# Optimization experiments

Measured on AMD Instinct MI355X. Metric: run time of the kernel, lower is better.

## Reference

```python
import jax, jax.numpy as jnp
import numpy as np

N_NODES = 100000
SAMPLES = 16


def setup_inputs() -> dict:
    key = jax.random.key(0)
    ks = jax.random.split(key, 9)
    x = jax.random.normal(ks[0], (N_NODES, 128), dtype=jnp.float32)
    neigh_idx = jax.random.randint(ks[1], (N_NODES, SAMPLES), 0, N_NODES)
    batch = jax.random.randint(ks[2], (8192,), 0, N_NODES)
    W1 = jax.random.normal(ks[3], (256, 128), dtype=jnp.float32) * 0.05
    b1 = jax.random.normal(ks[4], (128,), dtype=jnp.float32) * 0.05
    W2 = jax.random.normal(ks[5], (256, 128), dtype=jnp.float32) * 0.05
    b2 = jax.random.normal(ks[6], (128,), dtype=jnp.float32) * 0.05
    Wout = jax.random.normal(ks[7], (128, 64), dtype=jnp.float32) * 0.05
    bout = jax.random.normal(ks[8], (64,), dtype=jnp.float32) * 0.05
    return {"x": x, "neigh_idx": neigh_idx, "batch": batch,
            "W1": W1, "b1": b1, "W2": W2, "b2": b2,
            "Wout": Wout, "bout": bout}


def _sage_layer(h, neigh_idx, W, b):
    # h: [N, d]; gather sampled neighbors -> [N, S, d]; max-aggregate; concat-linear
    neigh = h[neigh_idx]                     # irregular gather, memory-bound core
    agg = jnp.max(neigh, axis=1)             # MaxAggregation over samples
    feats = jnp.concatenate([h, agg], axis=-1)  # [N, 2d]
    return feats @ W + b


def reference(x, neigh_idx, batch, W1, b1, W2, b2, Wout, bout):
    # layer 1: relu(Linear(concat(x, max_neigh(x))))
    h1 = jax.nn.relu(_sage_layer(x, neigh_idx, W1, b1))
    # layer 2 (== n_layers): Linear output (no relu) fed straight into proj_out
    h2 = _sage_layer(h1, neigh_idx, W2, b2)
    out = h2 @ Wout + bout                   # proj_out (Dropout is eval identity)
    return out[batch]
```

## Files before the change

kernel.cpp:

```cpp
#include <hip/hip_runtime.h>
#include <cmath>
#include <cstdint>

#define N_NODES 100000
#define SAMPLES 16
#define DIM 128
#define NBATCH 8192

#define FSTR 264
#define H2STR 132

typedef _Float16 half8 __attribute__((ext_vector_type(8)));
typedef float floatx4 __attribute__((ext_vector_type(4)));

__device__ __forceinline__ half8 h8max(half8 a, half8 b) {
    half8 r;
#pragma unroll
    for (int i = 0; i < 8; ++i) r[i] = (a[i] > b[i]) ? a[i] : b[i];
    return r;
}

__global__ __launch_bounds__(256) void setup_kernel(
    const float* __restrict__ x,
    const float* __restrict__ W1,
    const float* __restrict__ W2,
    const int* __restrict__ batch,
    const int* __restrict__ nidx,
    int* __restrict__ flags,
    _Float16* __restrict__ xh,
    _Float16* __restrict__ W1sw,
    _Float16* __restrict__ W2sw) {
    const int bid = blockIdx.x;
    if (bid < 6250) {
        const size_t base = ((size_t)bid * 256 + threadIdx.x) * 8;
        const float4* xp = (const float4*)(x + base);
        const float4 a = xp[0], b = xp[1];
        half8 v;
        v[0] = (_Float16)a.x; v[1] = (_Float16)a.y;
        v[2] = (_Float16)a.z; v[3] = (_Float16)a.w;
        v[4] = (_Float16)b.x; v[5] = (_Float16)b.y;
        v[6] = (_Float16)b.z; v[7] = (_Float16)b.w;
        *(half8*)(xh + base) = v;
    } else if (bid < 6282) {
        const int tid = (bid - 6250) * 256 + threadIdx.x;
        const int which = tid >> 12;
        const int r = tid & 4095;
        const int kb = r >> 9, nb = (r >> 6) & 7, lane = r & 63;
        const int q = lane >> 4, c = lane & 15;
        const float* W = which ? W2 : W1;
        _Float16* O = which ? W2sw : W1sw;
        const int k0 = kb * 32 + q * 8;
        const int n = nb * 16 + c;
        half8 v;
#pragma unroll
        for (int j = 0; j < 8; ++j) v[j] = (_Float16)W[(size_t)(k0 + j) * DIM + n];
        *(half8*)(O + (size_t)r * 8) = v;
    } else {
        const int j = (bid - 6282) * 256 + threadIdx.x;
        if (j < NBATCH) {
            const int b = batch[j];
            flags[b] = 1;
            const int* row = nidx + (size_t)b * SAMPLES;
#pragma unroll
            for (int s = 0; s < SAMPLES; ++s) flags[row[s]] = 1;
        }
    }
}

__global__ __launch_bounds__(256) void layer1_kernel(
    const _Float16* __restrict__ xh,
    const int* __restrict__ nidx,
    const _Float16* __restrict__ W1sw,
    const float* __restrict__ b1,
    const int* __restrict__ flags,
    _Float16* __restrict__ h1h) {
    const int t = threadIdx.x;
    const int g = t >> 4;
    const int cl = t & 15;
    const int i0 = blockIdx.x * 16;
    const int i = i0 + g;

    __shared__ __align__(16) _Float16 feats[16 * FSTR];

    const bool fi = (flags[i] == 1);
    if (fi) {
        const char* xb = (const char*)xh;
        const int cb = cl * 16;
        const half8 self = *(const half8*)(xb + (size_t)i * 256 + cb);
        const int4* ip = (const int4*)(nidx + (size_t)i * SAMPLES);
        const int4 a0 = ip[0], a1 = ip[1], a2 = ip[2], a3 = ip[3];
        int off[16];
        off[0]  = a0.x * 256 + cb; off[1]  = a0.y * 256 + cb;
        off[2]  = a0.z * 256 + cb; off[3]  = a0.w * 256 + cb;
        off[4]  = a1.x * 256 + cb; off[5]  = a1.y * 256 + cb;
        off[6]  = a1.z * 256 + cb; off[7]  = a1.w * 256 + cb;
        off[8]  = a2.x * 256 + cb; off[9]  = a2.y * 256 + cb;
        off[10] = a2.z * 256 + cb; off[11] = a2.w * 256 + cb;
        off[12] = a3.x * 256 + cb; off[13] = a3.y * 256 + cb;
        off[14] = a3.z * 256 + cb; off[15] = a3.w * 256 + cb;
        half8 v[16];
#pragma unroll
        for (int s = 0; s < 16; ++s) v[s] = *(const half8*)(xb + off[s]);
#pragma unroll
        for (int s = 0; s < 8; ++s) v[s] = h8max(v[s], v[s + 8]);
#pragma unroll
        for (int s = 0; s < 4; ++s) v[s] = h8max(v[s], v[s + 4]);
        const half8 mx = h8max(h8max(v[0], v[1]), h8max(v[2], v[3]));
        *(half8*)(feats + g * FSTR + cl * 8) = self;
        *(half8*)(feats + g * FSTR + DIM + cl * 8) = mx;
    } else {
        half8 z;
#pragma unroll
        for (int e = 0; e < 8; ++e) z[e] = (_Float16)0.f;
        *(half8*)(feats + g * FSTR + cl * 8) = z;
        *(half8*)(feats + g * FSTR + DIM + cl * 8) = z;
    }
    __syncthreads();

    const int wave = t >> 6;
    const int lane = t & 63;
    const int q = lane >> 4, c = lane & 15;
    const int nb0 = wave * 2;
    floatx4 acc[2];
    acc[0] = (floatx4){0.f, 0.f, 0.f, 0.f};
    acc[1] = (floatx4){0.f, 0.f, 0.f, 0.f};
#pragma unroll
    for (int kb = 0; kb < 8; ++kb) {
        const half8 a = *(const half8*)(feats + c * FSTR + kb * 32 + q * 8);
#pragma unroll
        for (int j = 0; j < 2; ++j) {
            const half8 b = *(const half8*)(W1sw + (size_t)((kb * 8 + nb0 + j) * 64 + lane) * 8);
            acc[j] = __builtin_amdgcn_mfma_f32_16x16x32_f16(a, b, acc[j], 0, 0, 0);
        }
    }

#pragma unroll
    for (int r = 0; r < 4; ++r) {
        const int node = i0 + q * 4 + r;
        if (flags[node] != 1) continue;
#pragma unroll
        for (int j = 0; j < 2; ++j) {
            const int n = (nb0 + j) * 16 + c;
            const float v = fmaxf(acc[j][r] + b1[n], 0.f);
            const _Float16 hv = (_Float16)v;
            __builtin_nontemporal_store(hv, h1h + (size_t)node * DIM + n);
        }
    }
}

__global__ __launch_bounds__(256) void layer2_kernel(
    const _Float16* __restrict__ h1h,
    const int* __restrict__ nidx,
    const int* __restrict__ batch,
    const _Float16* __restrict__ W2sw,
    const float* __restrict__ b2,
    const float* __restrict__ Wout,
    const float* __restrict__ bout,
    float* __restrict__ out) {
    const int t = threadIdx.x;
    const int wave = t >> 6;
    const int lane = t & 63;
    const int q = lane >> 4, c = lane & 15;
    const int w0 = blockIdx.x * 16;

    __shared__ __align__(16) _Float16 feats[16 * FSTR];
    __shared__ __align__(16) float h2s[16 * H2STR];

    {
        const int m = t >> 4;
        const int cl = t & 15;
        const int node = batch[w0 + m];
        const char* hb = (const char*)h1h;
        const int cb = cl * 16;
        const half8 self = *(const half8*)(hb + (size_t)node * 256 + cb);
        const int4* ip = (const int4*)(nidx + (size_t)node * SAMPLES);
        const int4 a0 = ip[0], a1 = ip[1], a2 = ip[2], a3 = ip[3];
        int off[16];
        off[0]  = a0.x * 256 + cb; off[1]  = a0.y * 256 + cb;
        off[2]  = a0.z * 256 + cb; off[3]  = a0.w * 256 + cb;
        off[4]  = a1.x * 256 + cb; off[5]  = a1.y * 256 + cb;
        off[6]  = a1.z * 256 + cb; off[7]  = a1.w * 256 + cb;
        off[8]  = a2.x * 256 + cb; off[9]  = a2.y * 256 + cb;
        off[10] = a2.z * 256 + cb; off[11] = a2.w * 256 + cb;
        off[12] = a3.x * 256 + cb; off[13] = a3.y * 256 + cb;
        off[14] = a3.z * 256 + cb; off[15] = a3.w * 256 + cb;
        half8 v[16];
#pragma unroll
        for (int s = 0; s < 16; ++s) v[s] = *(const half8*)(hb + off[s]);
#pragma unroll
        for (int s = 0; s < 8; ++s) v[s] = h8max(v[s], v[s + 8]);
#pragma unroll
        for (int s = 0; s < 4; ++s) v[s] = h8max(v[s], v[s + 4]);
        const half8 mx = h8max(h8max(v[0], v[1]), h8max(v[2], v[3]));
        *(half8*)(feats + m * FSTR + cl * 8) = self;
        *(half8*)(feats + m * FSTR + DIM + cl * 8) = mx;
    }
    __syncthreads();

    const int nb0 = wave * 2;
    floatx4 acc[2];
    acc[0] = (floatx4){0.f, 0.f, 0.f, 0.f};
    acc[1] = (floatx4){0.f, 0.f, 0.f, 0.f};
#pragma unroll
    for (int kb = 0; kb < 8; ++kb) {
        const half8 a = *(const half8*)(feats + c * FSTR + kb * 32 + q * 8);
#pragma unroll
        for (int j = 0; j < 2; ++j) {
            const half8 b = *(const half8*)(W2sw + (size_t)((kb * 8 + nb0 + j) * 64 + lane) * 8);
            acc[j] = __builtin_amdgcn_mfma_f32_16x16x32_f16(a, b, acc[j], 0, 0, 0);
        }
    }
#pragma unroll
    for (int j = 0; j < 2; ++j) {
        const int n = (nb0 + j) * 16 + c;
        const float bias = b2[n];
#pragma unroll
        for (int r = 0; r < 4; ++r)
            h2s[(q * 4 + r) * H2STR + n] = acc[j][r] + bias;
    }
    __syncthreads();

    float accs[4];
    const float bo = bout[lane];
#pragma unroll
    for (int r = 0; r < 4; ++r) accs[r] = bo;
    for (int k4 = 0; k4 < DIM; k4 += 4) {
        float wv[4];
#pragma unroll
        for (int j = 0; j < 4; ++j) wv[j] = Wout[(size_t)(k4 + j) * 64 + lane];
#pragma unroll
        for (int r = 0; r < 4; ++r) {
            const float4 f = *(const float4*)&h2s[(wave * 4 + r) * H2STR + k4];
            accs[r] += f.x * wv[0] + f.y * wv[1] + f.z * wv[2] + f.w * wv[3];
        }
    }
#pragma unroll
    for (int r = 0; r < 4; ++r)
        __builtin_nontemporal_store(accs[r], out + (size_t)(w0 + wave * 4 + r) * 64 + lane);
}

extern "C" void kernel_launch(void* const* d_in, const int* in_sizes, int n_in,
                              void* d_out, int out_size, void* d_ws, size_t ws_size,
                              hipStream_t stream) {
    const float* x    = (const float*)d_in[0];
    const int* nidx   = (const int*)d_in[1];
    const int* batch  = (const int*)d_in[2];
    const float* W1   = (const float*)d_in[3];
    const float* b1   = (const float*)d_in[4];
    const float* W2   = (const float*)d_in[5];
    const float* b2   = (const float*)d_in[6];
    const float* Wout = (const float*)d_in[7];
    const float* bout = (const float*)d_in[8];
    float* out        = (float*)d_out;

    int* flags      = (int*)d_ws;
    _Float16* W1sw  = (_Float16*)((char*)d_ws + 409600);
    _Float16* W2sw  = (_Float16*)((char*)d_ws + 475136);
    _Float16* xh    = (_Float16*)((char*)d_ws + 540672);
    _Float16* h1h   = (_Float16*)((char*)d_ws + 26140672);

    setup_kernel<<<6314, 256, 0, stream>>>(x, W1, W2, batch, nidx, flags, xh, W1sw, W2sw);
    layer1_kernel<<<N_NODES / 16, 256, 0, stream>>>(xh, nidx, W1sw, b1, flags, h1h);
    layer2_kernel<<<NBATCH / 16, 256, 0, stream>>>(h1h, nidx, batch, W2sw, b2, Wout, bout, out);
}
```

Baseline: 174.0 us.

## Split layer-1 gather into column-chunked kernel with chunk-major x layout

Stores the fp16 copy of x in a chunk-major layout (8 chunks of 16 features per node) and adds a separate gather kernel in which each block handles one feature chunk for 128 nodes. The working set per chunk (about 3.2MB) is meant to fit in cache, turning random 256-byte row gathers into cache-resident 32-byte accesses. The matmul kernel then reads the precomputed max-aggregate and overwrites the same buffer in place with h1. The cost is an extra kernel launch, an extra write and read of the aggregate buffer, and 8 re-reads of the neighbor index rows.

New measurement: 210.8 us. 21.2% more time.

```diff
diff --git a/kernel.cpp b/kernel.cpp
--- a/kernel.cpp
+++ b/kernel.cpp
@@ -12,6 +12,7 @@
 
 typedef _Float16 half8 __attribute__((ext_vector_type(8)));
 typedef float floatx4 __attribute__((ext_vector_type(4)));
+typedef int intx4 __attribute__((ext_vector_type(4)));
 
 __device__ __forceinline__ half8 h8max(half8 a, half8 b) {
     half8 r;
@@ -27,12 +28,15 @@
     const int* __restrict__ batch,
     const int* __restrict__ nidx,
     int* __restrict__ flags,
-    _Float16* __restrict__ xh,
+    _Float16* __restrict__ xc,
     _Float16* __restrict__ W1sw,
     _Float16* __restrict__ W2sw) {
     const int bid = blockIdx.x;
     if (bid < 6250) {
-        const size_t base = ((size_t)bid * 256 + threadIdx.x) * 8;
+        const int tid = bid * 256 + threadIdx.x;
+        const int node = tid >> 4;
+        const int cl = tid & 15;
+        const size_t base = (size_t)tid * 8;
         const float4* xp = (const float4*)(x + base);
         const float4 a = xp[0], b = xp[1];
         half8 v;
@@ -40,7 +44,8 @@
         v[2] = (_Float16)a.z; v[3] = (_Float16)a.w;
         v[4] = (_Float16)b.x; v[5] = (_Float16)b.y;
         v[6] = (_Float16)b.z; v[7] = (_Float16)b.w;
-        *(half8*)(xh + base) = v;
+        const int c = cl >> 1, h = cl & 1;
+        *(half8*)(xc + (size_t)c * (N_NODES * 16) + (size_t)node * 16 + h * 8) = v;
     } else if (bid < 6282) {
         const int tid = (bid - 6250) * 256 + threadIdx.x;
         const int which = tid >> 12;
@@ -67,13 +72,59 @@
     }
 }
 
-__global__ __launch_bounds__(256) void layer1_kernel(
-    const _Float16* __restrict__ xh,
+__global__ __launch_bounds__(256) void gather1_kernel(
+    const _Float16* __restrict__ xc,
     const int* __restrict__ nidx,
+    const int* __restrict__ flags,
+    _Float16* __restrict__ agg) {
+    const int bid = blockIdx.x;
+    const int c = bid & 7;
+    const int tile = bid >> 3;
+    const int t = threadIdx.x;
+    const int nl = t >> 1, h = t & 1;
+    const int node = tile * 128 + nl;
+    if (node >= N_NODES) return;
+    if (flags[node] != 1) return;
+
+    const _Float16* xcc = xc + (size_t)c * (N_NODES * 16) + h * 8;
+    const intx4* ip = (const intx4*)(nidx + (size_t)node * SAMPLES);
+    const intx4 a0 = __builtin_nontemporal_load(ip);
+    const intx4 a1 = __builtin_nontemporal_load(ip + 1);
+    const intx4 a2 = __builtin_nontemporal_load(ip + 2);
+    const intx4 a3 = __builtin_nontemporal_load(ip + 3);
+
+    half8 v[16];
+    v[0]  = *(const half8*)(xcc + a0[0] * 16);
+    v[1]  = *(const half8*)(xcc + a0[1] * 16);
+    v[2]  = *(const half8*)(xcc + a0[2] * 16);
+    v[3]  = *(const half8*)(xcc + a0[3] * 16);
+    v[4]  = *(const half8*)(xcc + a1[0] * 16);
+    v[5]  = *(const half8*)(xcc + a1[1] * 16);
+    v[6]  = *(const half8*)(xcc + a1[2] * 16);
+    v[7]  = *(const half8*)(xcc + a1[3] * 16);
+    v[8]  = *(const half8*)(xcc + a2[0] * 16);
+    v[9]  = *(const half8*)(xcc + a2[1] * 16);
+    v[10] = *(const half8*)(xcc + a2[2] * 16);
+    v[11] = *(const half8*)(xcc + a2[3] * 16);
+    v[12] = *(const half8*)(xcc + a3[0] * 16);
+    v[13] = *(const half8*)(xcc + a3[1] * 16);
+    v[14] = *(const half8*)(xcc + a3[2] * 16);
+    v[15] = *(const half8*)(xcc + a3[3] * 16);
+#pragma unroll
+    for (int s = 0; s < 8; ++s) v[s] = h8max(v[s], v[s + 8]);
+#pragma unroll
+    for (int s = 0; s < 4; ++s) v[s] = h8max(v[s], v[s + 4]);
+    const half8 mx = h8max(h8max(v[0], v[1]), h8max(v[2], v[3]));
+
+    __builtin_nontemporal_store(mx, (half8*)(agg + (size_t)node * DIM + c * 16 + h * 8));
+}
+
+__global__ __launch_bounds__(256) void layer1_mm_kernel(
+    const _Float16* __restrict__ xc,
     const _Float16* __restrict__ W1sw,
     const float* __restrict__ b1,
     const int* __restrict__ flags,
-    _Float16* __restrict__ h1h) {
+    _Float16* aggh) {
     const int t = threadIdx.x;
     const int g = t >> 4;
     const int cl = t & 15;
@@ -84,28 +135,9 @@
 
     const bool fi = (flags[i] == 1);
     if (fi) {
-        const char* xb = (const char*)xh;
-        const int cb = cl * 16;
-        const half8 self = *(const half8*)(xb + (size_t)i * 256 + cb);
-        const int4* ip = (const int4*)(nidx + (size_t)i * SAMPLES);
-        const int4 a0 = ip[0], a1 = ip[1], a2 = ip[2], a3 = ip[3];
-        int off[16];
-        off[0]  = a0.x * 256 + cb; off[1]  = a0.y * 256 + cb;
-        off[2]  = a0.z * 256 + cb; off[3]  = a0.w * 256 + cb;
-        off[4]  = a1.x * 256 + cb; off[5]  = a1.y * 256 + cb;
-        off[6]  = a1.z * 256 + cb; off[7]  = a1.w * 256 + cb;
-        off[8]  = a2.x * 256 + cb; off[9]  = a2.y * 256 + cb;
-        off[10] = a2.z * 256 + cb; off[11] = a2.w * 256 + cb;
-        off[12] = a3.x * 256 + cb; off[13] = a3.y * 256 + cb;
-        off[14] = a3.z * 256 + cb; off[15] = a3.w * 256 + cb;
-        half8 v[16];
-#pragma unroll
-        for (int s = 0; s < 16; ++s) v[s] = *(const half8*)(xb + off[s]);
-#pragma unroll
-        for (int s = 0; s < 8; ++s) v[s] = h8max(v[s], v[s + 8]);
-#pragma unroll
-        for (int s = 0; s < 4; ++s) v[s] = h8max(v[s], v[s + 4]);
-        const half8 mx = h8max(h8max(v[0], v[1]), h8max(v[2], v[3]));
+        const int c = cl >> 1, h = cl & 1;
+        const half8 self = *(const half8*)(xc + (size_t)c * (N_NODES * 16) + (size_t)i * 16 + h * 8);
+        const half8 mx = *(const half8*)(aggh + (size_t)i * DIM + cl * 8);
         *(half8*)(feats + g * FSTR + cl * 8) = self;
         *(half8*)(feats + g * FSTR + DIM + cl * 8) = mx;
     } else {
@@ -143,7 +175,7 @@
             const int n = (nb0 + j) * 16 + c;
             const float v = fmaxf(acc[j][r] + b1[n], 0.f);
             const _Float16 hv = (_Float16)v;
-            __builtin_nontemporal_store(hv, h1h + (size_t)node * DIM + n);
+            __builtin_nontemporal_store(hv, aggh + (size_t)node * DIM + n);
         }
     }
 }
@@ -256,10 +288,11 @@
     int* flags      = (int*)d_ws;
     _Float16* W1sw  = (_Float16*)((char*)d_ws + 409600);
     _Float16* W2sw  = (_Float16*)((char*)d_ws + 475136);
-    _Float16* xh    = (_Float16*)((char*)d_ws + 540672);
-    _Float16* h1h   = (_Float16*)((char*)d_ws + 26140672);
-
-    setup_kernel<<<6314, 256, 0, stream>>>(x, W1, W2, batch, nidx, flags, xh, W1sw, W2sw);
-    layer1_kernel<<<N_NODES / 16, 256, 0, stream>>>(xh, nidx, W1sw, b1, flags, h1h);
-    layer2_kernel<<<NBATCH / 16, 256, 0, stream>>>(h1h, nidx, batch, W2sw, b2, Wout, bout, out);
-}
+    _Float16* xc    = (_Float16*)((char*)d_ws + 540672);
+    _Float16* aggh  = (_Float16*)((char*)d_ws + 26140672);
+
+    setup_kernel<<<6314, 256, 0, stream>>>(x, W1, W2, batch, nidx, flags, xc, W1sw, W2sw);
+    gather1_kernel<<<782 * 8, 256, 0, stream>>>(xc, nidx, flags, aggh);
+    layer1_mm_kernel<<<N_NODES / 16, 256, 0, stream>>>(xc, W1sw, b1, flags, aggh);
+    layer2_kernel<<<NBATCH / 16, 256, 0, stream>>>(aggh, nidx, batch, W2sw, b2, Wout, bout, out);
+}
```

## Batch neighbor gathers in groups of four and widen layer2 to 512 threads

Applied to the files above, without the earlier changes.

Layer1's 16 neighbor gathers are now split into four groups of four, separated by scheduling barriers, with a running max. This lowers register pressure from holding all 16 half8 loads at once, at the cost of less memory-level parallelism per thread. Layer2 moves to 512 threads per block: each thread gathers half4 chunks, each wave runs one MFMA column tile instead of two, and each wave computes two output rows in the projection. This doubles the parallelism available per block for the batch gather.

New measurement: 170.0 us (median of 2 runs). 1.02x faster.

```diff
diff --git a/kernel.cpp b/kernel.cpp
--- a/kernel.cpp
+++ b/kernel.cpp
@@ -11,12 +11,20 @@
 #define H2STR 132
 
 typedef _Float16 half8 __attribute__((ext_vector_type(8)));
+typedef _Float16 half4 __attribute__((ext_vector_type(4)));
 typedef float floatx4 __attribute__((ext_vector_type(4)));
 
 __device__ __forceinline__ half8 h8max(half8 a, half8 b) {
     half8 r;
 #pragma unroll
     for (int i = 0; i < 8; ++i) r[i] = (a[i] > b[i]) ? a[i] : b[i];
+    return r;
+}
+
+__device__ __forceinline__ half4 h4max(half4 a, half4 b) {
+    half4 r;
+#pragma unroll
+    for (int i = 0; i < 4; ++i) r[i] = (a[i] > b[i]) ? a[i] : b[i];
     return r;
 }
 
@@ -98,16 +106,25 @@
         off[10] = a2.z * 256 + cb; off[11] = a2.w * 256 + cb;
         off[12] = a3.x * 256 + cb; off[13] = a3.y * 256 + cb;
         off[14] = a3.z * 256 + cb; off[15] = a3.w * 256 + cb;
-        half8 v[16];
-#pragma unroll
-        for (int s = 0; s < 16; ++s) v[s] = *(const half8*)(xb + off[s]);
-#pragma unroll
-        for (int s = 0; s < 8; ++s) v[s] = h8max(v[s], v[s + 8]);
-#pragma unroll
-        for (int s = 0; s < 4; ++s) v[s] = h8max(v[s], v[s + 4]);
-        const half8 mx = h8max(h8max(v[0], v[1]), h8max(v[2], v[3]));
+        half8 acc;
+        {
+            const half8 v0 = *(const half8*)(xb + off[0]);
+            const half8 v1 = *(const half8*)(xb + off[1]);
+            const half8 v2 = *(const half8*)(xb + off[2]);
+            const half8 v3 = *(const half8*)(xb + off[3]);
+            acc = h8max(h8max(v0, v1), h8max(v2, v3));
+        }
+#pragma unroll
+        for (int bp = 1; bp < 4; ++bp) {
+            __builtin_amdgcn_sched_barrier(0);
+            const half8 v0 = *(const half8*)(xb + off[4 * bp]);
+            const half8 v1 = *(const half8*)(xb + off[4 * bp + 1]);
+            const half8 v2 = *(const half8*)(xb + off[4 * bp + 2]);
+            const half8 v3 = *(const half8*)(xb + off[4 * bp + 3]);
+            acc = h8max(acc, h8max(h8max(v0, v1), h8max(v2, v3)));
+        }
         *(half8*)(feats + g * FSTR + cl * 8) = self;
-        *(half8*)(feats + g * FSTR + DIM + cl * 8) = mx;
+        *(half8*)(feats + g * FSTR + DIM + cl * 8) = acc;
     } else {
         half8 z;
 #pragma unroll
@@ -148,7 +165,7 @@
     }
 }
 
-__global__ __launch_bounds__(256) void layer2_kernel(
+__global__ __launch_bounds__(512) void layer2_kernel(
     const _Float16* __restrict__ h1h,
     const int* __restrict__ nidx,
     const int* __restrict__ batch,
@@ -167,12 +184,12 @@
     __shared__ __align__(16) float h2s[16 * H2STR];
 
     {
-        const int m = t >> 4;
-        const int cl = t & 15;
+        const int m = t >> 5;
+        const int cl = t & 31;
         const int node = batch[w0 + m];
         const char* hb = (const char*)h1h;
-        const int cb = cl * 16;
-        const half8 self = *(const half8*)(hb + (size_t)node * 256 + cb);
+        const int cb = cl * 8;
+        const half4 self = *(const half4*)(hb + (size_t)node * 256 + cb);
         const int4* ip = (const int4*)(nidx + (size_t)node * SAMPLES);
         const int4 a0 = ip[0], a1 = ip[1], a2 = ip[2], a3 = ip[3];
         int off[16];
@@ -184,59 +201,62 @@
         off[10] = a2.z * 256 + cb; off[11] = a2.w * 256 + cb;
         off[12] = a3.x * 256 + cb; off[13] = a3.y * 256 + cb;
         off[14] = a3.z * 256 + cb; off[15] = a3.w * 256 + cb;
-        half8 v[16];
-#pragma unroll
-        for (int s = 0; s < 16; ++s) v[s] = *(const half8*)(hb + off[s]);
-#pragma unroll
-        for (int s = 0; s < 8; ++s) v[s] = h8max(v[s], v[s + 8]);
-#pragma unroll
-        for (int s = 0; s < 4; ++s) v[s] = h8max(v[s], v[s + 4]);
-        const half8 mx = h8max(h8max(v[0], v[1]), h8max(v[2], v[3]));
-        *(half8*)(feats + m * FSTR + cl * 8) = self;
-        *(half8*)(feats + m * FSTR + DIM + cl * 8) = mx;
+        half4 acc;
+        {
+            const half4 v0 = *(const half4*)(hb + off[0]);
+            const half4 v1 = *(const half4*)(hb + off[1]);
+            const half4 v2 = *(const half4*)(hb + off[2]);
+            const half4 v3 = *(const half4*)(hb + off[3]);
+            acc = h4max(h4max(v0, v1), h4max(v2, v3));
+        }
+#pragma unroll
+        for (int bp = 1; bp < 4; ++bp) {
+            __builtin_amdgcn_sched_barrier(0);
+            const half4 v0 = *(const half4*)(hb + off[4 * bp]);
+            const half4 v1 = *(const half4*)(hb + off[4 * bp + 1]);
+            const half4 v2 = *(const half4*)(hb + off[4 * bp + 2]);
+            const half4 v3 = *(const half4*)(hb + off[4 * bp + 3]);
+            acc = h4max(acc, h4max(h4max(v0, v1), h4max(v2, v3)));
+        }
+        *(half4*)(feats + m * FSTR + cl * 4) = self;
+        *(half4*)(feats + m * FSTR + DIM + cl * 4) = acc;
     }
     __syncthreads();
 
-    const int nb0 = wave * 2;
-    floatx4 acc[2];
-    acc[0] = (floatx4){0.f, 0.f, 0.f, 0.f};
-    acc[1] = (floatx4){0.f, 0.f, 0.f, 0.f};
+    floatx4 acc;
+    acc = (floatx4){0.f, 0.f, 0.f, 0.f};
 #pragma unroll
     for (int kb = 0; kb < 8; ++kb) {
         const half8 a = *(const half8*)(feats + c * FSTR + kb * 32 + q * 8);
-#pragma unroll
-        for (int j = 0; j < 2; ++j) {
-            const half8 b = *(const half8*)(W2sw + (size_t)((kb * 8 + nb0 + j) * 64 + lane) * 8);
-            acc[j] = __builtin_amdgcn_mfma_f32_16x16x32_f16(a, b, acc[j], 0, 0, 0);
-        }
-    }
-#pragma unroll
-    for (int j = 0; j < 2; ++j) {
-        const int n = (nb0 + j) * 16 + c;
+        const half8 b = *(const half8*)(W2sw + (size_t)((kb * 8 + wave) * 64 + lane) * 8);
+        acc = __builtin_amdgcn_mfma_f32_16x16x32_f16(a, b, acc, 0, 0, 0);
+    }
+    {
+        const int n = wave * 16 + c;
         const float bias = b2[n];
 #pragma unroll
         for (int r = 0; r < 4; ++r)
-            h2s[(q * 4 + r) * H2STR + n] = acc[j][r] + bias;
+            h2s[(q * 4 + r) * H2STR + n] = acc[r] + bias;
     }
     __syncthreads();
 
-    float accs[4];
+    float accs[2];
     const float bo = bout[lane];
 #pragma unroll
-    for (int r = 0; r < 4; ++r) accs[r] = bo;
+    for (int r = 0; r < 2; ++r) accs[r] = bo;
     for (int k4 = 0; k4 < DIM; k4 += 4) {
         float wv[4];
 #pragma unroll
         for (int j = 0; j < 4; ++j) wv[j] = Wout[(size_t)(k4 + j) * 64 + lane];
 #pragma unroll
-        for (int r = 0; r < 4; ++r) {
-            const float4 f = *(const float4*)&h2s[(wave * 4 + r) * H2STR + k4];
+        for (int r = 0; r < 2; ++r) {
+            const float4 f = *(const float4*)&h2s[(wave * 2 + r) * H2STR + k4];
             accs[r] += f.x * wv[0] + f.y * wv[1] + f.z * wv[2] + f.w * wv[3];
         }
     }
 #pragma unroll
-    for (int r = 0; r < 4; ++r)
-        __builtin_nontemporal_store(accs[r], out + (size_t)(w0 + wave * 4 + r) * 64 + lane);
+    for (int r = 0; r < 2; ++r)
+        __builtin_nontemporal_store(accs[r], out + (size_t)(w0 + wave * 2 + r) * 64 + lane);
 }
 
 extern "C" void kernel_launch(void* const* d_in, const int* in_sizes, int n_in,
@@ -261,5 +281,5 @@
 
     setup_kernel<<<6314, 256, 0, stream>>>(x, W1, W2, batch, nidx, flags, xh, W1sw, W2sw);
     layer1_kernel<<<N_NODES / 16, 256, 0, stream>>>(xh, nidx, W1sw, b1, flags, h1h);
-    layer2_kernel<<<NBATCH / 16, 256, 0, stream>>>(h1h, nidx, batch, W2sw, b2, Wout, bout, out);
-}
+    layer2_kernel<<<NBATCH / 16, 512, 0, stream>>>(h1h, nidx, batch, W2sw, b2, Wout, bout, out);
+}
```
